# Performance work log

Hardware: AMD Instinct MI355X
Metric: run time of the kernel (lower is better)

## Reference

```python
import jax, jax.numpy as jnp
import numpy as np
import math

B, S, D, H = 2, 2048, 1024, 16
HD = D // H  # head dim = 64


def setup_inputs() -> dict:
    key = jax.random.key(0)
    ks = jax.random.split(key, 8)
    scale = 1.0 / math.sqrt(D)
    return {
        "x": jax.random.normal(ks[0], (B, S, D), dtype=jnp.float32),
        "mask": jax.random.randint(ks[1], (B, S, S), 0, 2).astype(bool),
        "Wq": jax.random.normal(ks[2], (D, D), dtype=jnp.float32) * scale,
        "bq": jax.random.normal(ks[3], (D,), dtype=jnp.float32) * 0.01,
        "Wk": jax.random.normal(ks[4], (D, D), dtype=jnp.float32) * scale,
        "bk": jax.random.normal(ks[5], (D,), dtype=jnp.float32) * 0.01,
        "Wv": jax.random.normal(ks[6], (D, D), dtype=jnp.float32) * scale,
        "bv": jax.random.normal(ks[7], (D,), dtype=jnp.float32) * 0.01,
    }


def reference(x, mask, Wq, bq, Wk, bk, Wv, bv):
    # Linear projections (weights stored as [in, out])
    q = x @ Wq + bq  # [B,S,D]
    k = x @ Wk + bk
    v = x @ Wv + bv
    # split heads -> [B,H,S,HD]
    q = q.reshape(B, S, H, HD).transpose(0, 2, 1, 3)
    k = k.reshape(B, S, H, HD).transpose(0, 2, 1, 3)
    v = v.reshape(B, S, H, HD).transpose(0, 2, 1, 3)
    scores = jnp.einsum("bhqd,bhkd->bhqk", q, k) / jnp.sqrt(jnp.float32(HD))
    # Faithful to the source: masked_fill_(mask, -inf) is immediately
    # overwritten by masked_fill_(mask, 0), so masked positions end up 0
    # BEFORE the softmax (a quirk of the original module).
    scores = jnp.where(mask[:, None, :, :], 0.0, scores)
    attn = jax.nn.softmax(scores, axis=-1)  # dropout=0.0 (eval)
    out = jnp.einsum("bhqk,bhkd->bhqd", attn, v)
    return out.transpose(0, 2, 1, 3).reshape(B, S, D)
```

## Files before the change

kernel.cpp:

```cpp
#include <hip/hip_runtime.h>
#include <cstdint>
#include <cstddef>

static constexpr int B_ = 2, S_ = 2048, D_ = 1024, H_ = 16, HD_ = 64;

typedef float f32x4 __attribute__((ext_vector_type(4)));
typedef short bf16x8 __attribute__((ext_vector_type(8)));

__device__ __forceinline__ unsigned short f2bf(float f) {
    union { float f; unsigned int u; } v; v.f = f;
    unsigned int r = v.u + 0x7FFFu + ((v.u >> 16) & 1u);
    return (unsigned short)(r >> 16);
}

__device__ __forceinline__ unsigned pack2bf(float a, float b) {
    union { float f; unsigned u; } va, vb; va.f = a; vb.f = b;
    unsigned ra = va.u + 0x7FFFu + ((va.u >> 16) & 1u);
    unsigned rb = vb.u + 0x7FFFu + ((vb.u >> 16) & 1u);
    return __builtin_amdgcn_perm(rb, ra, 0x07060302u);
}

__device__ __forceinline__ void gload_lds16(const void* g, void* l) {
    __builtin_amdgcn_global_load_lds(
        (const __attribute__((address_space(1))) void*)g,
        (__attribute__((address_space(3))) void*)l, 16, 0, 0);
}

__global__ __launch_bounds__(256)
void prep(const float* __restrict__ x, unsigned short* __restrict__ xo,
          const int* __restrict__ m, unsigned char* __restrict__ mo,
          const float* __restrict__ Wq, const float* __restrict__ Wk,
          const float* __restrict__ Wv, unsigned short* __restrict__ wt) {
    __shared__ unsigned short Ts[64][72];
    const int bid = blockIdx.x, t = threadIdx.x;
    if (bid < 2048) {
        size_t i = ((size_t)bid * 256 + t) * 8;
        float4 a = *(const float4*)(x + i);
        float4 c = *(const float4*)(x + i + 4);
        uint4 r;
        r.x = pack2bf(a.x, a.y); r.y = pack2bf(a.z, a.w);
        r.z = pack2bf(c.x, c.y); r.w = pack2bf(c.z, c.w);
        *(uint4*)(xo + i) = r;
    } else if (bid < 4096) {
        size_t i = ((size_t)(bid - 2048) * 256 + t) * 16;
        uint4 r;
        unsigned w[4];
        #pragma unroll
        for (int g = 0; g < 4; ++g) {
            int4 v = *(const int4*)(m + i + g * 4);
            w[g] = (v.x ? 0xFFu : 0u) | (v.y ? 0xFF00u : 0u) |
                   (v.z ? 0xFF0000u : 0u) | (v.w ? 0xFF000000u : 0u);
        }
        r.x = w[0]; r.y = w[1]; r.z = w[2]; r.w = w[3];
        *(uint4*)(mo + i) = r;
    } else {
        const int tid = bid - 4096;
        const int mat = tid >> 8, tile = tid & 255;
        const float* __restrict__ W = (mat == 0) ? Wq : (mat == 1) ? Wk : Wv;
        unsigned short* __restrict__ o = wt + (size_t)mat * D_ * D_;
        const int n0 = (tile & 15) * 64, k0 = (tile >> 4) * 64;
        {
            const int nl = t & 63, kb = t >> 6;
            #pragma unroll
            for (int i = 0; i < 16; ++i) {
                int k = kb + i * 4;
                Ts[nl][k] = f2bf(W[(size_t)(k0 + k) * D_ + n0 + nl]);
            }
        }
        __syncthreads();
        {
            const int kl = t & 63, nb = t >> 6;
            #pragma unroll
            for (int i = 0; i < 16; ++i) {
                int n = nb + i * 4;
                o[(size_t)(n0 + n) * D_ + k0 + kl] = Ts[n][kl];
            }
        }
    }
}

__global__ __launch_bounds__(512)
void qkv_gemm(const unsigned short* __restrict__ xb, const unsigned short* __restrict__ wt,
              const float* __restrict__ bq, const float* __restrict__ bk,
              const float* __restrict__ bv,
              unsigned short* __restrict__ qo, unsigned short* __restrict__ ko,
              unsigned short* __restrict__ vto) {
    const int bx = blockIdx.x;
    const int by = blockIdx.y;
    const int mat = bx >> 3;
    const int ncol0 = (bx & 7) * 128;
    const float* __restrict__ bias = (mat == 0) ? bq : (mat == 1) ? bk : bv;
    const unsigned short* __restrict__ Wm = wt + (size_t)mat * D_ * D_;

    __shared__ unsigned short As[2][128 * 32];
    __shared__ unsigned short Bs[2][128 * 32];

    const int t = threadIdx.x;
    const int w = t >> 6, lane = t & 63;
    const int l15 = lane & 15, quad = lane >> 4;
    const int mw = (w >> 2) * 64, nw = (w & 3) * 32;
    const int rowBase = by * 128;

    const int r16 = lane >> 2;
    const int sslot = lane & 3;
    const int sg = (sslot ^ ((r16 >> 1) & 3)) * 8;
    const int srow = w * 16 + r16;
    const int rcol = (quad ^ ((l15 >> 1) & 3)) * 8;

    f32x4 acc[4][2] = {};

    gload_lds16(xb + (size_t)(rowBase + srow) * D_ + sg, &As[0][w * 16 * 32]);
    gload_lds16(Wm + (size_t)(ncol0 + srow) * D_ + sg, &Bs[0][w * 16 * 32]);

    for (int it = 0; it < 32; ++it) {
        const int cur = it & 1;
        __syncthreads();
        if (it + 1 < 32) {
            const int ktn = (it + 1) * 32;
            gload_lds16(xb + (size_t)(rowBase + srow) * D_ + ktn + sg,
                        &As[cur ^ 1][w * 16 * 32]);
            gload_lds16(Wm + (size_t)(ncol0 + srow) * D_ + ktn + sg,
                        &Bs[cur ^ 1][w * 16 * 32]);
        }

        bf16x8 a[4], b[2];
        #pragma unroll
        for (int i = 0; i < 4; ++i)
            a[i] = *(const bf16x8*)&As[cur][(mw + i * 16 + l15) * 32 + rcol];
        #pragma unroll
        for (int j = 0; j < 2; ++j)
            b[j] = *(const bf16x8*)&Bs[cur][(nw + j * 16 + l15) * 32 + rcol];
        #pragma unroll
        for (int i = 0; i < 4; ++i)
            #pragma unroll
            for (int j = 0; j < 2; ++j)
                acc[i][j] = __builtin_amdgcn_mfma_f32_16x16x32_bf16(a[i], b[j], acc[i][j], 0, 0, 0);
    }

    if (mat < 2) {
        unsigned short* __restrict__ O = (mat == 0) ? qo : ko;
        const float osc = (mat == 0) ? 0.18033688011112443f : 1.0f;
        #pragma unroll
        for (int j = 0; j < 2; ++j) {
            const int col = ncol0 + nw + j * 16 + l15;
            const float bb = bias[col];
            #pragma unroll
            for (int i = 0; i < 4; ++i)
                #pragma unroll
                for (int r = 0; r < 4; ++r) {
                    const int m = rowBase + mw + i * 16 + quad * 4 + r;
                    O[(size_t)m * D_ + col] = f2bf((acc[i][j][r] + bb) * osc);
                }
        }
    } else {
        #pragma unroll
        for (int j = 0; j < 2; ++j) {
            const int col = ncol0 + nw + j * 16 + l15;
            const float bb = bias[col];
            const int hh = col >> 6, hd = col & 63;
            #pragma unroll
            for (int i = 0; i < 4; ++i) {
                const int m0 = rowBase + mw + i * 16 + quad * 4;
                const int bg = m0 >> 11, s0 = m0 & 2047;
                ushort4 pk;
                pk.x = f2bf(acc[i][j][0] + bb);
                pk.y = f2bf(acc[i][j][1] + bb);
                pk.z = f2bf(acc[i][j][2] + bb);
                pk.w = f2bf(acc[i][j][3] + bb);
                *(ushort4*)&vto[(((size_t)bg * H_ + hh) * HD_ + hd) * S_ + s0] = pk;
            }
        }
    }
}

__global__ __launch_bounds__(1024, 8)
void attn_mfma(const unsigned short* __restrict__ qmat,
               const unsigned short* __restrict__ kmat,
               const unsigned short* __restrict__ vtg,
               const unsigned char* __restrict__ msk, float* __restrict__ out) {
    const int h = blockIdx.x, qt = blockIdx.y, b = blockIdx.z;
    const int t = threadIdx.x, w = t >> 6, lane = t & 63;
    const int l15 = lane & 15, quad = lane >> 4;
    const int q0 = qt * 128;

    __shared__ __align__(16) char smem[49152];
    unsigned short* const Ksm = (unsigned short*)smem;
    unsigned short* const Vsm = (unsigned short*)(smem + 16384);
    unsigned short* const Psm = (unsigned short*)(smem + 32768);

    const size_t bh = (size_t)b * S_ * D_ + (size_t)h * HD_;
    const unsigned short* __restrict__ qp = qmat + bh;
    const unsigned short* __restrict__ kp = kmat + bh;
    const unsigned short* __restrict__ vp = vtg + ((size_t)b * H_ + h) * HD_ * S_;
    const unsigned char* __restrict__ mb = msk + (size_t)b * S_ * S_;

    const int rs = lane >> 3, sslot = lane & 7;
    const int sg = (sslot ^ rs) * 8;
    const int sr8 = (w & 7) * 8 + rs;
    const bool stK = (w < 8);

    const int wq = w >> 1;
    const int kw = (w & 1) * 32;
    const int qr = wq * 16 + l15;
    const int sw7 = l15 & 7;

    bf16x8 qfr[2];
    #pragma unroll
    for (int kst = 0; kst < 2; ++kst)
        qfr[kst] = *(const bf16x8*)(qp + (size_t)(q0 + qr) * D_ + kst * 32 + quad * 8);

    f32x4 accO[4] = {};
    f32x4 lsA = {};
    bf16x8 ones;
    #pragma unroll
    for (int i = 0; i < 8; ++i) ones[i] = (short)0x3F80;

    if (stK) gload_lds16(kp + (size_t)sr8 * D_ + sg, Ksm + (w & 7) * 8 * 64);
    else     gload_lds16(vp + (size_t)sr8 * S_ + sg, Vsm + (w & 7) * 8 * 64);

    for (int it = 0; it < 32; ++it) {
        const int cur = it & 1;
        const int kt = it * 64;
        __syncthreads();

        unsigned mu[2];
        {
            const unsigned char* __restrict__ mrow = mb + (size_t)(q0 + qr) * S_ + kt + kw;
            mu[0] = *(const unsigned*)(mrow + quad * 4);
            mu[1] = *(const unsigned*)(mrow + 16 + quad * 4);
        }

        if (it + 1 < 32) {
            const int ktn = kt + 64;
            if (stK) gload_lds16(kp + (size_t)(ktn + sr8) * D_ + sg,
                                 Ksm + (cur ^ 1) * 4096 + (w & 7) * 8 * 64);
            else     gload_lds16(vp + (size_t)sr8 * S_ + ktn + sg,
                                 Vsm + (cur ^ 1) * 4096 + (w & 7) * 8 * 64);
        }

        f32x4 sc[2] = {};
        #pragma unroll
        for (int kst = 0; kst < 2; ++kst) {
            bf16x8 kfr[2];
            #pragma unroll
            for (int mt = 0; mt < 2; ++mt) {
                const int R = kw + mt * 16 + l15;
                kfr[mt] = *(const bf16x8*)&Ksm[cur * 4096 + R * 64 +
                                               (((kst * 4 + quad) ^ sw7) * 8)];
            }
            __builtin_amdgcn_s_setprio(1);
            #pragma unroll
            for (int mt = 0; mt < 2; ++mt)
                sc[mt] = __builtin_amdgcn_mfma_f32_16x16x32_bf16(kfr[mt], qfr[kst], sc[mt], 0, 0, 0);
            __builtin_amdgcn_s_setprio(0);
        }

        #pragma unroll
        for (int mt = 0; mt < 2; ++mt) {
            const int mtg = (w & 1) * 2 + mt;
            unsigned p0 = pack2bf(__builtin_amdgcn_exp2f(sc[mt][0]),
                                  __builtin_amdgcn_exp2f(sc[mt][1]));
            unsigned p1 = pack2bf(__builtin_amdgcn_exp2f(sc[mt][2]),
                                  __builtin_amdgcn_exp2f(sc[mt][3]));
            const unsigned m0 = __builtin_amdgcn_perm(0u, mu[mt], 0x01010000u);
            const unsigned m1 = __builtin_amdgcn_perm(0u, mu[mt], 0x03030202u);
            p0 = (m0 & 0x3F803F80u) | (~m0 & p0);
            p1 = (m1 & 0x3F803F80u) | (~m1 & p1);
            uint2 pk2; pk2.x = p0; pk2.y = p1;
            *(uint2*)((char*)Psm + qr * 128 +
                      (((2 * mtg + (quad >> 1)) ^ sw7) * 16) + (quad & 1) * 8) = pk2;
        }

        {
            const int kst = w & 1;
            bf16x8 vfr[4];
            #pragma unroll
            for (int dt = 0; dt < 4; ++dt) {
                const int R = dt * 16 + l15;
                vfr[dt] = *(const bf16x8*)&Vsm[cur * 4096 + R * 64 +
                                               (((kst * 4 + quad) ^ sw7) * 8)];
            }
            bf16x8 pfr = *(const bf16x8*)((const char*)Psm + qr * 128 +
                                          (((kst * 4 + quad) ^ sw7) * 16));
            __builtin_amdgcn_s_setprio(1);
            #pragma unroll
            for (int dt = 0; dt < 4; ++dt)
                accO[dt] = __builtin_amdgcn_mfma_f32_16x16x32_bf16(pfr, vfr[dt], accO[dt], 0, 0, 0);
            lsA = __builtin_amdgcn_mfma_f32_16x16x32_bf16(pfr, ones, lsA, 0, 0, 0);
            __builtin_amdgcn_s_setprio(0);
        }
    }

    __syncthreads();
    float* const Red = (float*)smem;
    const int pidx = (wq * 64 + lane) * 20;
    if (w & 1) {
        #pragma unroll
        for (int dt = 0; dt < 4; ++dt)
            *(f32x4*)&Red[pidx + dt * 4] = accO[dt];
        *(f32x4*)&Red[pidx + 16] = lsA;
    }
    __syncthreads();
    if (!(w & 1)) {
        #pragma unroll
        for (int dt = 0; dt < 4; ++dt)
            accO[dt] += *(const f32x4*)&Red[pidx + dt * 4];
        lsA += *(const f32x4*)&Red[pidx + 16];

        float* __restrict__ ob = out + ((size_t)b * S_ + q0) * D_ + (size_t)h * HD_;
        #pragma unroll
        for (int r = 0; r < 4; ++r) {
            const float inv = 1.0f / lsA[r];
            const int row = wq * 16 + quad * 4 + r;
            #pragma unroll
            for (int dt = 0; dt < 4; ++dt)
                ob[(size_t)row * D_ + dt * 16 + l15] = accO[dt][r] * inv;
        }
    }
}

extern "C" void kernel_launch(void* const* d_in, const int* in_sizes, int n_in,
                              void* d_out, int out_size, void* d_ws, size_t ws_size,
                              hipStream_t stream) {
    (void)in_sizes; (void)n_in; (void)out_size; (void)ws_size;
    const float* x    = (const float*)d_in[0];
    const int*   mask = (const int*)d_in[1];
    const float* Wq   = (const float*)d_in[2];
    const float* bq   = (const float*)d_in[3];
    const float* Wk   = (const float*)d_in[4];
    const float* bk   = (const float*)d_in[5];
    const float* Wv   = (const float*)d_in[6];
    const float* bv   = (const float*)d_in[7];
    float* out = (float*)d_out;

    const size_t M1 = (size_t)1024 * 1024;
    unsigned short* xb  = (unsigned short*)d_ws;
    unsigned short* wtb = xb + 4 * M1;
    unsigned short* qb  = wtb + 3 * M1;
    unsigned short* kb  = qb + 4 * M1;
    unsigned short* vtb = kb + 4 * M1;
    unsigned char*  mk  = (unsigned char*)(vtb + 4 * M1);

    prep<<<4864, 256, 0, stream>>>(x, xb, mask, mk, Wq, Wk, Wv, wtb);
    qkv_gemm<<<dim3(24, 32), 512, 0, stream>>>(xb, wtb, bq, bk, bv, qb, kb, vtb);
    attn_mfma<<<dim3(16, 16, 2), 1024, 0, stream>>>(qb, kb, vtb, mk, out);
}
```

Before: 257.4 us.

## Halve attention block to 512 threads with two query subtiles per wave

Each wave in the attention kernel now handles two 16-row query subtiles instead of one. The block drops from 1024 to 512 threads, and every wave loads both a K and a V slice. K fragments read from LDS are reused across the two query subtiles, which cuts LDS reads per MFMA and halves the number of waves per block. The cost is more registers per thread (twice the accumulators, scores and Q fragments) and fewer waves available to hide latency.

```diff
diff --git a/kernel.cpp b/kernel.cpp
--- a/kernel.cpp
+++ b/kernel.cpp
@@ -173,7 +173,7 @@
     }
 }
 
-__global__ __launch_bounds__(1024, 8)
+__global__ __launch_bounds__(512, 4)
 void attn_mfma(const unsigned short* __restrict__ qmat,
                const unsigned short* __restrict__ kmat,
                const unsigned short* __restrict__ vtg,
@@ -196,83 +196,93 @@
 
     const int rs = lane >> 3, sslot = lane & 7;
     const int sg = (sslot ^ rs) * 8;
-    const int sr8 = (w & 7) * 8 + rs;
-    const bool stK = (w < 8);
-
-    const int wq = w >> 1;
+    const int srow = w * 8 + rs;
+
+    const int qs = w >> 1;
     const int kw = (w & 1) * 32;
-    const int qr = wq * 16 + l15;
+    const int kst = w & 1;
     const int sw7 = l15 & 7;
 
-    bf16x8 qfr[2];
+    bf16x8 qfr[2][2];
     #pragma unroll
-    for (int kst = 0; kst < 2; ++kst)
-        qfr[kst] = *(const bf16x8*)(qp + (size_t)(q0 + qr) * D_ + kst * 32 + quad * 8);
-
-    f32x4 accO[4] = {};
-    f32x4 lsA = {};
+    for (int nt = 0; nt < 2; ++nt)
+        #pragma unroll
+        for (int dk = 0; dk < 2; ++dk)
+            qfr[nt][dk] = *(const bf16x8*)(qp +
+                (size_t)(q0 + qs * 32 + nt * 16 + l15) * D_ + dk * 32 + quad * 8);
+
+    f32x4 accO[2][4] = {};
+    f32x4 lsA[2] = {};
     bf16x8 ones;
     #pragma unroll
     for (int i = 0; i < 8; ++i) ones[i] = (short)0x3F80;
 
-    if (stK) gload_lds16(kp + (size_t)sr8 * D_ + sg, Ksm + (w & 7) * 8 * 64);
-    else     gload_lds16(vp + (size_t)sr8 * S_ + sg, Vsm + (w & 7) * 8 * 64);
+    gload_lds16(kp + (size_t)srow * D_ + sg, Ksm + w * 8 * 64);
+    gload_lds16(vp + (size_t)srow * S_ + sg, Vsm + w * 8 * 64);
 
     for (int it = 0; it < 32; ++it) {
         const int cur = it & 1;
         const int kt = it * 64;
         __syncthreads();
 
-        unsigned mu[2];
-        {
-            const unsigned char* __restrict__ mrow = mb + (size_t)(q0 + qr) * S_ + kt + kw;
-            mu[0] = *(const unsigned*)(mrow + quad * 4);
-            mu[1] = *(const unsigned*)(mrow + 16 + quad * 4);
+        unsigned mu[2][2];
+        #pragma unroll
+        for (int nt = 0; nt < 2; ++nt) {
+            const unsigned char* __restrict__ mrow =
+                mb + (size_t)(q0 + qs * 32 + nt * 16 + l15) * S_ + kt + kw;
+            mu[nt][0] = *(const unsigned*)(mrow + quad * 4);
+            mu[nt][1] = *(const unsigned*)(mrow + 16 + quad * 4);
         }
 
         if (it + 1 < 32) {
             const int ktn = kt + 64;
-            if (stK) gload_lds16(kp + (size_t)(ktn + sr8) * D_ + sg,
-                                 Ksm + (cur ^ 1) * 4096 + (w & 7) * 8 * 64);
-            else     gload_lds16(vp + (size_t)sr8 * S_ + ktn + sg,
-                                 Vsm + (cur ^ 1) * 4096 + (w & 7) * 8 * 64);
-        }
-
-        f32x4 sc[2] = {};
-        #pragma unroll
-        for (int kst = 0; kst < 2; ++kst) {
+            gload_lds16(kp + (size_t)(ktn + srow) * D_ + sg,
+                        Ksm + (cur ^ 1) * 4096 + w * 8 * 64);
+            gload_lds16(vp + (size_t)srow * S_ + ktn + sg,
+                        Vsm + (cur ^ 1) * 4096 + w * 8 * 64);
+        }
+
+        f32x4 sc[2][2] = {};
+        #pragma unroll
+        for (int dk = 0; dk < 2; ++dk) {
             bf16x8 kfr[2];
             #pragma unroll
             for (int mt = 0; mt < 2; ++mt) {
                 const int R = kw + mt * 16 + l15;
                 kfr[mt] = *(const bf16x8*)&Ksm[cur * 4096 + R * 64 +
-                                               (((kst * 4 + quad) ^ sw7) * 8)];
+                                               (((dk * 4 + quad) ^ sw7) * 8)];
             }
             __builtin_amdgcn_s_setprio(1);
             #pragma unroll
-            for (int mt = 0; mt < 2; ++mt)
-                sc[mt] = __builtin_amdgcn_mfma_f32_16x16x32_bf16(kfr[mt], qfr[kst], sc[mt], 0, 0, 0);
+            for (int nt = 0; nt < 2; ++nt)
+                #pragma unroll
+                for (int mt = 0; mt < 2; ++mt)
+                    sc[nt][mt] = __builtin_amdgcn_mfma_f32_16x16x32_bf16(
+                        kfr[mt], qfr[nt][dk], sc[nt][mt], 0, 0, 0);
             __builtin_amdgcn_s_setprio(0);
         }
 
         #pragma unroll
-        for (int mt = 0; mt < 2; ++mt) {
-            const int mtg = (w & 1) * 2 + mt;
-            unsigned p0 = pack2bf(__builtin_amdgcn_exp2f(sc[mt][0]),
-                                  __builtin_amdgcn_exp2f(sc[mt][1]));
-            unsigned p1 = pack2bf(__builtin_amdgcn_exp2f(sc[mt][2]),
-                                  __builtin_amdgcn_exp2f(sc[mt][3]));
-            const unsigned m0 = __builtin_amdgcn_perm(0u, mu[mt], 0x01010000u);
-            const unsigned m1 = __builtin_amdgcn_perm(0u, mu[mt], 0x03030202u);
-            p0 = (m0 & 0x3F803F80u) | (~m0 & p0);
-            p1 = (m1 & 0x3F803F80u) | (~m1 & p1);
-            uint2 pk2; pk2.x = p0; pk2.y = p1;
-            *(uint2*)((char*)Psm + qr * 128 +
-                      (((2 * mtg + (quad >> 1)) ^ sw7) * 16) + (quad & 1) * 8) = pk2;
+        for (int nt = 0; nt < 2; ++nt) {
+            const int qr = qs * 32 + nt * 16 + l15;
+            #pragma unroll
+            for (int mt = 0; mt < 2; ++mt) {
+                const int mtg = kst * 2 + mt;
+                unsigned p0 = pack2bf(__builtin_amdgcn_exp2f(sc[nt][mt][0]),
+                                      __builtin_amdgcn_exp2f(sc[nt][mt][1]));
+                unsigned p1 = pack2bf(__builtin_amdgcn_exp2f(sc[nt][mt][2]),
+                                      __builtin_amdgcn_exp2f(sc[nt][mt][3]));
+                const unsigned m0 = __builtin_amdgcn_perm(0u, mu[nt][mt], 0x01010000u);
+                const unsigned m1 = __builtin_amdgcn_perm(0u, mu[nt][mt], 0x03030202u);
+                p0 = (m0 & 0x3F803F80u) | (~m0 & p0);
+                p1 = (m1 & 0x3F803F80u) | (~m1 & p1);
+                uint2 pk2; pk2.x = p0; pk2.y = p1;
+                *(uint2*)((char*)Psm + qr * 128 +
+                          (((2 * mtg + (quad >> 1)) ^ sw7) * 16) + (quad & 1) * 8) = pk2;
+            }
         }
 
         {
-            const int kst = w & 1;
             bf16x8 vfr[4];
             #pragma unroll
             for (int dt = 0; dt < 4; ++dt) {
@@ -280,41 +290,53 @@
                 vfr[dt] = *(const bf16x8*)&Vsm[cur * 4096 + R * 64 +
                                                (((kst * 4 + quad) ^ sw7) * 8)];
             }
-            bf16x8 pfr = *(const bf16x8*)((const char*)Psm + qr * 128 +
-                                          (((kst * 4 + quad) ^ sw7) * 16));
-            __builtin_amdgcn_s_setprio(1);
-            #pragma unroll
-            for (int dt = 0; dt < 4; ++dt)
-                accO[dt] = __builtin_amdgcn_mfma_f32_16x16x32_bf16(pfr, vfr[dt], accO[dt], 0, 0, 0);
-            lsA = __builtin_amdgcn_mfma_f32_16x16x32_bf16(pfr, ones, lsA, 0, 0, 0);
-            __builtin_amdgcn_s_setprio(0);
+            #pragma unroll
+            for (int nt = 0; nt < 2; ++nt) {
+                const int qr = qs * 32 + nt * 16 + l15;
+                bf16x8 pfr = *(const bf16x8*)((const char*)Psm + qr * 128 +
+                                              (((kst * 4 + quad) ^ sw7) * 16));
+                __builtin_amdgcn_s_setprio(1);
+                #pragma unroll
+                for (int dt = 0; dt < 4; ++dt)
+                    accO[nt][dt] = __builtin_amdgcn_mfma_f32_16x16x32_bf16(
+                        pfr, vfr[dt], accO[nt][dt], 0, 0, 0);
+                lsA[nt] = __builtin_amdgcn_mfma_f32_16x16x32_bf16(pfr, ones, lsA[nt], 0, 0, 0);
+                __builtin_amdgcn_s_setprio(0);
+            }
         }
     }
 
     __syncthreads();
     float* const Red = (float*)smem;
-    const int pidx = (wq * 64 + lane) * 20;
     if (w & 1) {
         #pragma unroll
-        for (int dt = 0; dt < 4; ++dt)
-            *(f32x4*)&Red[pidx + dt * 4] = accO[dt];
-        *(f32x4*)&Red[pidx + 16] = lsA;
+        for (int nt = 0; nt < 2; ++nt) {
+            const int pidx = ((qs * 2 + nt) * 64 + lane) * 20;
+            #pragma unroll
+            for (int dt = 0; dt < 4; ++dt)
+                *(f32x4*)&Red[pidx + dt * 4] = accO[nt][dt];
+            *(f32x4*)&Red[pidx + 16] = lsA[nt];
+        }
     }
     __syncthreads();
     if (!(w & 1)) {
-        #pragma unroll
-        for (int dt = 0; dt < 4; ++dt)
-            accO[dt] += *(const f32x4*)&Red[pidx + dt * 4];
-        lsA += *(const f32x4*)&Red[pidx + 16];
-
         float* __restrict__ ob = out + ((size_t)b * S_ + q0) * D_ + (size_t)h * HD_;
         #pragma unroll
-        for (int r = 0; r < 4; ++r) {
-            const float inv = 1.0f / lsA[r];
-            const int row = wq * 16 + quad * 4 + r;
+        for (int nt = 0; nt < 2; ++nt) {
+            const int pidx = ((qs * 2 + nt) * 64 + lane) * 20;
             #pragma unroll
             for (int dt = 0; dt < 4; ++dt)
-                ob[(size_t)row * D_ + dt * 16 + l15] = accO[dt][r] * inv;
+                accO[nt][dt] += *(const f32x4*)&Red[pidx + dt * 4];
+            lsA[nt] += *(const f32x4*)&Red[pidx + 16];
+
+            #pragma unroll
+            for (int r = 0; r < 4; ++r) {
+                const float inv = 1.0f / lsA[nt][r];
+                const int row = qs * 32 + nt * 16 + quad * 4 + r;
+                #pragma unroll
+                for (int dt = 0; dt < 4; ++dt)
+                    ob[(size_t)row * D_ + dt * 16 + l15] = accO[nt][dt][r] * inv;
+            }
         }
     }
 }
@@ -343,5 +365,5 @@
 
     prep<<<4864, 256, 0, stream>>>(x, xb, mask, mk, Wq, Wk, Wv, wtb);
     qkv_gemm<<<dim3(24, 32), 512, 0, stream>>>(xb, wtb, bq, bk, bv, qb, kb, vtb);
-    attn_mfma<<<dim3(16, 16, 2), 1024, 0, stream>>>(qb, kb, vtb, mk, out);
-}
+    attn_mfma<<<dim3(16, 16, 2), 512, 0, stream>>>(qb, kb, vtb, mk, out);
+}
```

Result: faster. 210.3 us, median of 2 (-18.3%).
